# Optimization experiments

Measured on AMD Instinct MI355X. Metric: run time of the kernel, lower is better.

Reference implementation:

```python
import jax, jax.numpy as jnp
import numpy as np

# Routing structure from the torch module
GT0 = [[0,1,0,0,1,0],[0,1,0,0,0,1],[0,0,1,0,1,0],[0,0,1,0,0,1],[0,0,0,1,1,0],[0,0,0,1,0,1]]
NCLS = 6
K = 1  # top-k

def _expert_pairs():
    # For class i, expert index m = 1+(j-1)*5+(k-1) maps to atom1[j-1] -> atom2[k-1].
    pairs = []
    for i in range(NCLS):
        p = [(j - 1, k - 1) for j in range(1, 6) for k in range(1, 6)
             if j != k and GT0[i][j] == 1 and GT0[i][k] == 1]
        pairs.append(p)
    return pairs

PAIRS = _expert_pairs()  # each class has exactly 2 (atom1, atom2) pairs

B, P, D, H = 64, 256, 768, 3072

def setup_inputs() -> dict:
    key = jax.random.key(0)
    ks = jax.random.split(key, 8)
    s = 0.02
    x = jax.random.normal(ks[0], (B, NCLS + P, D), dtype=jnp.float32)
    mids = jax.random.randint(ks[1], (B,), 0, 6)
    moe0_W1 = jax.random.normal(ks[2], (D, H), dtype=jnp.float32) * s
    moe0_b1 = jnp.zeros((H,), jnp.float32)
    moe0_W2 = jax.random.normal(ks[3], (H, D), dtype=jnp.float32) * s
    moe0_b2 = jnp.zeros((D,), jnp.float32)
    A1_W = jax.random.normal(ks[4], (5, D, H), dtype=jnp.float32) * s  # atom1 linears
    A1_b = jnp.zeros((5, H), jnp.float32)
    A2_W = jax.random.normal(ks[5], (5, H, D), dtype=jnp.float32) * s  # atom2 linears
    A2_b = jnp.zeros((5, D), jnp.float32)
    G_W = jax.random.normal(ks[6], (NCLS, D, 2), dtype=jnp.float32) * s  # per-class gates (2 experts each, no bias)
    return {"x": x, "moe0_W1": moe0_W1, "moe0_b1": moe0_b1, "moe0_W2": moe0_W2,
            "moe0_b2": moe0_b2, "A1_W": A1_W, "A1_b": A1_b, "A2_W": A2_W,
            "A2_b": A2_b, "G_W": G_W, "mids": mids}

def _gelu(t):
    return jax.nn.gelu(t, approximate=False)  # torch nn.GELU default = erf

def reference(x, moe0_W1, moe0_b1, moe0_W2, moe0_b2, A1_W, A1_b, A2_W, A2_b, G_W, mids):
    cls_tokens = x[:, :NCLS]          # [B, 6, D]
    patch_tokens = x[:, NCLS:]        # [B, P, D]
    patch_out = _gelu(patch_tokens @ moe0_W1 + moe0_b1) @ moe0_W2 + moe0_b2  # [B, P, D]
    cls_outs = []
    for i in range(NCLS):
        tok = cls_tokens[:, i]        # [B, D]
        eouts = [ _gelu(tok @ A1_W[a] + A1_b[a]) @ A2_W[c] + A2_b[c] for (a, c) in PAIRS[i] ]
        out = jnp.stack(eouts, axis=-1)                 # [B, D, E=2]
        gate = jax.nn.softmax(tok @ G_W[i], axis=-1)    # [B, E]
        # top-k masking (k=1 < E=2): keep gates strictly above the (k+1)-th largest
        thr = jnp.sort(gate, axis=-1)[..., -(K + 1)]    # [B]
        mask = (gate > thr[..., None]).astype(gate.dtype)
        g = gate * mask
        g = g / jnp.clip(jnp.sum(g, axis=-1, keepdims=True), 1e-6)
        cls_outs.append(jnp.sum(out * g[:, None, :], axis=-1))  # [B, D]
    cls_out = jnp.stack(cls_outs, axis=1)               # [B, 6, D]
    return jnp.concatenate([cls_out, patch_out], axis=1)  # [B, 6+P, D]
```

## Files before the change

### kernel.cpp

```cpp
#include <hip/hip_runtime.h>
#include <hip/hip_bf16.h>

#define DD 768
#define HH 3072
#define BB 64
#define TT 262

typedef __bf16 bf16x8 __attribute__((ext_vector_type(8)));
typedef float f32x4 __attribute__((ext_vector_type(4)));
typedef unsigned short u16;
typedef unsigned int u32;

__device__ __constant__ int A_FIRST[12]  = {0,3, 0,4, 1,3, 1,4, 2,3, 2,4};
__device__ __constant__ int A_SECOND[12] = {3,0, 4,0, 3,1, 4,1, 3,2, 4,2};

__device__ __forceinline__ float gelu_f(float x) {
  float n2t = x * fmaf(x * x, -0.0713548163f, -1.5957691216f);
  return x * __builtin_amdgcn_rcpf(1.0f + __expf(n2t));
}

__device__ __forceinline__ u16 f2bf(float x) {
  u32 u = __builtin_bit_cast(u32, x);
  return (u16)((u + 0x7fffu + ((u >> 16) & 1u)) >> 16);
}

__device__ __forceinline__ void load_lds16(const void* g, void* l) {
  __builtin_amdgcn_global_load_lds(
      (const __attribute__((address_space(1))) void*)g,
      (__attribute__((address_space(3))) void*)l,
      16, 0, 0);
}

__global__ __launch_bounds__(256)
void preproc(const float* __restrict__ x,
             const float* __restrict__ W1, const float* __restrict__ A1W,
             const float* __restrict__ W2, const float* __restrict__ A2W,
             const float* __restrict__ GW,
             __hip_bfloat16* __restrict__ xb,
             __hip_bfloat16* __restrict__ W1t, __hip_bfloat16* __restrict__ A1t,
             __hip_bfloat16* __restrict__ W2t, __hip_bfloat16* __restrict__ A2t,
             int* __restrict__ sel) {
  __shared__ __hip_bfloat16 tile[32][33];
  const int bx = blockIdx.x;
  const int tid = threadIdx.x;
  if (bx < 12576) {
    int i = bx * 256 + tid;
    float4 v = ((const float4*)x)[i];
    union { u16 s[4]; uint2 d; } pk;
    pk.s[0] = f2bf(v.x); pk.s[1] = f2bf(v.y); pk.s[2] = f2bf(v.z); pk.s[3] = f2bf(v.w);
    *(uint2*)((u16*)xb + (size_t)i * 4) = pk.d;
  } else if (bx < 40224) {
    int R, C;
    const float* ip;
    __hip_bfloat16* op;
    int t;
    if (bx < 26400) {
      t = bx - 12576; R = DD; C = HH;
      int z = t / 2304; t %= 2304;
      ip = z ? (A1W + (size_t)(z - 1) * DD * HH) : W1;
      op = z ? (A1t + (size_t)(z - 1) * DD * HH) : W1t;
    } else {
      t = bx - 26400; R = HH; C = DD;
      int z = t / 2304; t %= 2304;
      ip = z ? (A2W + (size_t)(z - 1) * DD * HH) : W2;
      op = z ? (A2t + (size_t)(z - 1) * DD * HH) : W2t;
    }
    int ctiles = C >> 5;
    int c0 = (t % ctiles) * 32, r0 = (t / ctiles) * 32;
    int tx = tid & 31, ty = tid >> 5;
#pragma unroll
    for (int s = 0; s < 4; ++s) {
      int rr = ty * 4 + s;
      tile[rr][tx] = __float2bfloat16(ip[(size_t)(r0 + rr) * C + c0 + tx]);
    }
    __syncthreads();
#pragma unroll
    for (int s = 0; s < 4; ++s) {
      int cc = ty * 4 + s;
      op[(size_t)(c0 + cc) * R + r0 + tx] = tile[tx][cc];
    }
  } else {
    int unit = (bx - 40224) * 4 + (tid >> 6);
    int lane = tid & 63;
    int b = unit & 63, i = unit >> 6;
    const float* tok = x + (size_t)(b * TT + i) * DD;
    const float* g = GW + (size_t)i * DD * 2;
    float p0 = 0.f, p1 = 0.f;
    for (int k = lane; k < DD; k += 64) {
      float tv = tok[k];
      p0 += tv * g[k * 2 + 0];
      p1 += tv * g[k * 2 + 1];
    }
#pragma unroll
    for (int o = 32; o; o >>= 1) { p0 += __shfl_xor(p0, o); p1 += __shfl_xor(p1, o); }
    if (lane == 0) sel[i * 64 + b] = (p0 > p1) ? 0 : ((p1 > p0) ? 1 : 2);
  }
}

template <int BM, int BN, int MODE>
__device__ __forceinline__
void gemm_body(char* __restrict__ smem, int bx,
               const __hip_bfloat16* __restrict__ A,
               const __hip_bfloat16* __restrict__ Bw,
               const float* __restrict__ bias,
               void* __restrict__ Out,
               const int* __restrict__ sel) {
  constexpr int KDIM = (MODE == 0 || MODE == 2) ? DD : HH;
  constexpr int KITERS = KDIM / 64;
  constexpr int WAVES_M = (BM == 128) ? 2 : 1;
  constexpr int WAVES_N = 4 / WAVES_M;
  constexpr int MT = BM / (16 * WAVES_M);
  constexpr int NT = BN / (16 * WAVES_N);
  constexpr int CHA = BM / 32;
  constexpr int CHB = BN / 32;

  char* As = smem;
  char* Bs = smem + BM * 128;

  const int tid = threadIdx.x;
  const int lane = tid & 63;
  const int wave = tid >> 6;
  const int q = lane >> 4;
  const int r = lane & 15;
  const int wave_m = wave / WAVES_N;
  const int wave_n = wave % WAVES_N;

  int m0 = 0, n0, combo = 0, cls_i = 0;
  const __hip_bfloat16* Bp = Bw;
  const float* biasp = bias;
  if constexpr (MODE == 0) {
    int chunk = bx / 192, local = bx % 192;
    int nb = local / 16, mloc = local % 16;
    m0 = (chunk * 16 + mloc) * BM;
    n0 = nb * BN;
  } else if constexpr (MODE == 1) {
    int chunk = bx / 96, local = bx % 96;
    int nb = local / 16, mloc = local % 16;
    m0 = (chunk * 16 + mloc) * BM;
    n0 = nb * BN;
  } else if constexpr (MODE == 2) {
    n0 = (bx % 24) * BN;
    combo = bx / 24;
    cls_i = combo >> 1;
    int e = A_FIRST[combo];
    Bp = Bw + (size_t)e * DD * HH;
    biasp = bias + e * HH;
  } else {
    n0 = (bx % 6) * BN;
    combo = bx / 6;
    cls_i = combo >> 1;
    int e = A_SECOND[combo];
    Bp = Bw + (size_t)e * DD * HH;
    biasp = bias + e * DD;
  }

  const int trow = tid >> 3;
  const int sw = ((tid & 7) ^ (trow & 7)) << 4;
  size_t a_row_off;
  if constexpr (MODE == 0) {
    int m = m0 + trow;
    a_row_off = (size_t)((m >> 8) * TT + 6 + (m & 255)) * DD * 2;
  } else if constexpr (MODE == 1) {
    a_row_off = (size_t)(m0 + trow) * HH * 2;
  } else if constexpr (MODE == 2) {
    a_row_off = (size_t)(trow * TT + cls_i) * DD * 2;
  } else {
    a_row_off = (size_t)(combo * 64 + trow) * HH * 2;
  }
  const char* gA0 = (const char*)A + a_row_off + sw;
  const char* gB0 = (const char*)Bp + (size_t)(n0 + trow) * KDIM * 2 + sw;
  constexpr size_t ASTR = (size_t)32 * ((MODE == 0) ? DD : (MODE == 2) ? TT * DD : HH) * 2;
  constexpr size_t BSTR = (size_t)32 * KDIM * 2;
  const int wave_base = (tid & ~63) * 16;

  f32x4 acc[MT][NT];
#pragma unroll
  for (int i_ = 0; i_ < MT; ++i_)
#pragma unroll
    for (int j_ = 0; j_ < NT; ++j_) acc[i_][j_] = (f32x4){0.f, 0.f, 0.f, 0.f};

  const char* a_rd = As + (wave_m * (MT * 16) + r) * 128;
  const char* b_rd = Bs + (wave_n * (NT * 16) + r) * 128;
  const int sa = ((q ^ (r & 7)) << 4);

  for (int kt = 0; kt < KITERS; ++kt) {
#pragma unroll
    for (int u = 0; u < CHA; ++u) load_lds16(gA0 + u * ASTR, As + u * 4096 + wave_base);
#pragma unroll
    for (int u = 0; u < CHB; ++u) load_lds16(gB0 + u * BSTR, Bs + u * 4096 + wave_base);
    gA0 += 128;
    gB0 += 128;
    __syncthreads();
#pragma unroll
    for (int t = 0; t < 2; ++t) {
      const int so = sa ^ (t << 6);
      bf16x8 af[MT], bf[NT];
#pragma unroll
      for (int i_ = 0; i_ < MT; ++i_) af[i_] = *(const bf16x8*)(a_rd + i_ * 2048 + so);
#pragma unroll
      for (int j_ = 0; j_ < NT; ++j_) bf[j_] = *(const bf16x8*)(b_rd + j_ * 2048 + so);
#pragma unroll
      for (int i_ = 0; i_ < MT; ++i_)
#pragma unroll
        for (int j_ = 0; j_ < NT; ++j_)
          acc[i_][j_] = __builtin_amdgcn_mfma_f32_16x16x32_bf16(bf[j_], af[i_], acc[i_][j_], 0, 0, 0);
    }
    __syncthreads();
  }

#pragma unroll
  for (int i_ = 0; i_ < MT; ++i_) {
    int m_g = m0 + wave_m * (MT * 16) + i_ * 16 + r;
#pragma unroll
    for (int j_ = 0; j_ < NT; ++j_) {
      int nb = n0 + wave_n * (NT * 16) + j_ * 16 + q * 4;
      f32x4 v = acc[i_][j_];
      f32x4 bb = *(const f32x4*)(biasp + nb);
      v += bb;
      if constexpr (MODE == 0) {
        union { u16 s[4]; uint2 d; } pk;
#pragma unroll
        for (int rg = 0; rg < 4; ++rg) pk.s[rg] = f2bf(gelu_f(v[rg]));
        *(uint2*)((u16*)Out + (size_t)m_g * HH + nb) = pk.d;
      } else if constexpr (MODE == 1) {
        int b = m_g >> 8, p = m_g & 255;
        *(f32x4*)((float*)Out + (size_t)(b * TT + 6 + p) * DD + nb) = v;
      } else if constexpr (MODE == 2) {
        union { u16 s[4]; uint2 d; } pk;
#pragma unroll
        for (int rg = 0; rg < 4; ++rg) pk.s[rg] = f2bf(gelu_f(v[rg]));
        *(uint2*)((u16*)Out + (size_t)(combo * 64 + m_g) * HH + nb) = pk.d;
      } else {
        int s = sel[cls_i * 64 + m_g];
        int j = combo & 1;
        float* dst = (float*)Out + (size_t)(m_g * TT + cls_i) * DD + nb;
        if (s == j) {
          *(f32x4*)dst = v;
        } else if (j == 0 && s == 2) {
          *(f32x4*)dst = (f32x4){0.f, 0.f, 0.f, 0.f};
        }
      }
    }
  }
}

__global__ __launch_bounds__(256, 2)
void mega1(const __hip_bfloat16* __restrict__ xb, const __hip_bfloat16* __restrict__ W1t,
           const float* __restrict__ b1, __hip_bfloat16* __restrict__ hid,
           const __hip_bfloat16* __restrict__ A1t, const float* __restrict__ A1b,
           __hip_bfloat16* __restrict__ hcls) {
  __shared__ __align__(16) char smem[(128 + 256) * 128];
  int bx = blockIdx.x;
  if (bx < 1536) gemm_body<128, 256, 0>(smem, bx, xb, W1t, b1, hid, nullptr);
  else           gemm_body<64, 128, 2>(smem, bx - 1536, xb, A1t, A1b, hcls, nullptr);
}

__global__ __launch_bounds__(256, 2)
void mega2(const __hip_bfloat16* __restrict__ hid, const __hip_bfloat16* __restrict__ W2t,
           const float* __restrict__ b2, float* __restrict__ out,
           const __hip_bfloat16* __restrict__ hcls, const __hip_bfloat16* __restrict__ A2t,
           const float* __restrict__ A2b, const int* __restrict__ sel) {
  __shared__ __align__(16) char smem[(128 + 128) * 128];
  int bx = blockIdx.x;
  if (bx < 768) gemm_body<128, 128, 1>(smem, bx, hid, W2t, b2, out, nullptr);
  else          gemm_body<64, 128, 3>(smem, bx - 768, hcls, A2t, A2b, out, sel);
}

extern "C" void kernel_launch(void* const* d_in, const int* in_sizes, int n_in,
                              void* d_out, int out_size, void* d_ws, size_t ws_size,
                              hipStream_t stream) {
  const float* x   = (const float*)d_in[0];
  const float* W1  = (const float*)d_in[1];
  const float* b1  = (const float*)d_in[2];
  const float* W2  = (const float*)d_in[3];
  const float* b2  = (const float*)d_in[4];
  const float* A1W = (const float*)d_in[5];
  const float* A1b = (const float*)d_in[6];
  const float* A2W = (const float*)d_in[7];
  const float* A2b = (const float*)d_in[8];
  const float* GW  = (const float*)d_in[9];
  float* out = (float*)d_out;

  char* ws = (char*)d_ws;
  __hip_bfloat16* xb   = (__hip_bfloat16*)(ws + 0);
  __hip_bfloat16* W1t  = (__hip_bfloat16*)(ws + 25755648);
  __hip_bfloat16* W2t  = (__hip_bfloat16*)(ws + 30474240);
  __hip_bfloat16* A1t  = (__hip_bfloat16*)(ws + 35192832);
  __hip_bfloat16* A2t  = (__hip_bfloat16*)(ws + 58785792);
  __hip_bfloat16* hcls = (__hip_bfloat16*)(ws + 82378752);
  int* sel             = (int*)(ws + 87097344);
  __hip_bfloat16* hid  = (__hip_bfloat16*)(ws + 87099136);

  preproc<<<40320, 256, 0, stream>>>(x, W1, A1W, W2, A2W, GW, xb, W1t, A1t, W2t, A2t, sel);
  mega1<<<1824, 256, 0, stream>>>(xb, W1t, b1, hid, A1t, A1b, hcls);
  mega2<<<840, 256, 0, stream>>>(hid, W2t, b2, out, hcls, A2t, A2b, sel);
}
```

Before: 403.0 us.

## Use 256x256 double-buffered GEMM tiles with interleaved LDS staging and MFMA

Replaces the generic GEMM body for the two large patch GEMMs with a 512-thread, 256x256-tile kernel. It double-buffers LDS (128KB) and interleaves the next K-slab's global-to-LDS loads with MFMA groups, using vmcnt waits, raw barriers and s_setprio. The goal is to hide global load latency and raise data reuse per tile. The small class-token GEMMs get their own 512-thread path. The trade-offs: the second GEMM now launches only 192 large tiles, which may leave CUs idle, and the large LDS footprint limits occupancy to one block per CU.

```diff
diff --git a/kernel.cpp b/kernel.cpp
--- a/kernel.cpp
+++ b/kernel.cpp
@@ -30,6 +30,9 @@
       (__attribute__((address_space(3))) void*)l,
       16, 0, 0);
 }
+
+#define VMCNT(n) asm volatile("s_waitcnt vmcnt(" #n ")")
+#define BAR() __builtin_amdgcn_s_barrier()
 
 __global__ __launch_bounds__(256)
 void preproc(const float* __restrict__ x,
@@ -97,173 +100,265 @@
   }
 }
 
-template <int BM, int BN, int MODE>
+template <int MH, int KS>
+__device__ __forceinline__ void rd_a(bf16x8 (&af)[4], const char* ab, int a_rd0) {
+#pragma unroll
+  for (int ii = 0; ii < 4; ++ii)
+    af[ii] = *(const bf16x8*)(ab + MH * 16384 + ii * 2048 + (a_rd0 ^ (KS << 6)));
+}
+template <int KS>
+__device__ __forceinline__ void rd_b(bf16x8 (&bf)[4], const char* bb, int b_rd0) {
+#pragma unroll
+  for (int j = 0; j < 4; ++j)
+    bf[j] = *(const bf16x8*)(bb + (j >> 1) * 16384 + (j & 1) * 2048 + (b_rd0 ^ (KS << 6)));
+}
+template <int MH>
+__device__ __forceinline__ void mma16(f32x4 (&acc)[8][4], const bf16x8 (&af)[4], const bf16x8 (&bf)[4]) {
+  __builtin_amdgcn_s_setprio(1);
+#pragma unroll
+  for (int ii = 0; ii < 4; ++ii)
+#pragma unroll
+    for (int j = 0; j < 4; ++j)
+      acc[MH * 4 + ii][j] =
+          __builtin_amdgcn_mfma_f32_16x16x32_bf16(bf[j], af[ii], acc[MH * 4 + ii][j], 0, 0, 0);
+  __builtin_amdgcn_s_setprio(0);
+}
+
+template <int MODE>
 __device__ __forceinline__
-void gemm_body(char* __restrict__ smem, int bx,
-               const __hip_bfloat16* __restrict__ A,
-               const __hip_bfloat16* __restrict__ Bw,
-               const float* __restrict__ bias,
-               void* __restrict__ Out,
-               const int* __restrict__ sel) {
-  constexpr int KDIM = (MODE == 0 || MODE == 2) ? DD : HH;
-  constexpr int KITERS = KDIM / 64;
-  constexpr int WAVES_M = (BM == 128) ? 2 : 1;
-  constexpr int WAVES_N = 4 / WAVES_M;
-  constexpr int MT = BM / (16 * WAVES_M);
-  constexpr int NT = BN / (16 * WAVES_N);
-  constexpr int CHA = BM / 32;
-  constexpr int CHB = BN / 32;
+void gemm_big(char* __restrict__ smem, int bx,
+              const __hip_bfloat16* __restrict__ A,
+              const __hip_bfloat16* __restrict__ Bw,
+              const float* __restrict__ bias,
+              void* __restrict__ Out) {
+  constexpr int KDIM = (MODE == 0) ? DD : HH;
+  constexpr int KT = KDIM / 64;
+  constexpr int KB = KDIM * 2;
 
   char* As = smem;
-  char* Bs = smem + BM * 128;
+  char* Bs = smem + 65536;
 
   const int tid = threadIdx.x;
   const int lane = tid & 63;
-  const int wave = tid >> 6;
   const int q = lane >> 4;
   const int r = lane & 15;
-  const int wave_m = wave / WAVES_N;
-  const int wave_n = wave % WAVES_N;
-
-  int m0 = 0, n0, combo = 0, cls_i = 0;
-  const __hip_bfloat16* Bp = Bw;
-  const float* biasp = bias;
+  const int wave = tid >> 6;
+  const int wave_m = wave >> 2;
+  const int wave_n = wave & 3;
+
+  int m0, n0;
   if constexpr (MODE == 0) {
     int chunk = bx / 192, local = bx % 192;
-    int nb = local / 16, mloc = local % 16;
-    m0 = (chunk * 16 + mloc) * BM;
-    n0 = nb * BN;
-  } else if constexpr (MODE == 1) {
-    int chunk = bx / 96, local = bx % 96;
-    int nb = local / 16, mloc = local % 16;
-    m0 = (chunk * 16 + mloc) * BM;
-    n0 = nb * BN;
-  } else if constexpr (MODE == 2) {
-    n0 = (bx % 24) * BN;
-    combo = bx / 24;
-    cls_i = combo >> 1;
-    int e = A_FIRST[combo];
-    Bp = Bw + (size_t)e * DD * HH;
-    biasp = bias + e * HH;
+    m0 = (chunk * 16 + local % 16) * 256;
+    n0 = (local / 16) * 256;
   } else {
-    n0 = (bx % 6) * BN;
-    combo = bx / 6;
-    cls_i = combo >> 1;
-    int e = A_SECOND[combo];
-    Bp = Bw + (size_t)e * DD * HH;
-    biasp = bias + e * DD;
+    m0 = (bx % 64) * 256;
+    n0 = (bx / 64) * 256;
   }
 
   const int trow = tid >> 3;
   const int sw = ((tid & 7) ^ (trow & 7)) << 4;
-  size_t a_row_off;
-  if constexpr (MODE == 0) {
-    int m = m0 + trow;
-    a_row_off = (size_t)((m >> 8) * TT + 6 + (m & 255)) * DD * 2;
-  } else if constexpr (MODE == 1) {
-    a_row_off = (size_t)(m0 + trow) * HH * 2;
-  } else if constexpr (MODE == 2) {
-    a_row_off = (size_t)(trow * TT + cls_i) * DD * 2;
-  } else {
-    a_row_off = (size_t)(combo * 64 + trow) * HH * 2;
-  }
-  const char* gA0 = (const char*)A + a_row_off + sw;
-  const char* gB0 = (const char*)Bp + (size_t)(n0 + trow) * KDIM * 2 + sw;
-  constexpr size_t ASTR = (size_t)32 * ((MODE == 0) ? DD : (MODE == 2) ? TT * DD : HH) * 2;
-  constexpr size_t BSTR = (size_t)32 * KDIM * 2;
-  const int wave_base = (tid & ~63) * 16;
-
-  f32x4 acc[MT][NT];
-#pragma unroll
-  for (int i_ = 0; i_ < MT; ++i_)
-#pragma unroll
-    for (int j_ = 0; j_ < NT; ++j_) acc[i_][j_] = (f32x4){0.f, 0.f, 0.f, 0.f};
-
-  const char* a_rd = As + (wave_m * (MT * 16) + r) * 128;
-  const char* b_rd = Bs + (wave_n * (NT * 16) + r) * 128;
-  const int sa = ((q ^ (r & 7)) << 4);
-
-  for (int kt = 0; kt < KITERS; ++kt) {
-#pragma unroll
-    for (int u = 0; u < CHA; ++u) load_lds16(gA0 + u * ASTR, As + u * 4096 + wave_base);
-#pragma unroll
-    for (int u = 0; u < CHB; ++u) load_lds16(gB0 + u * BSTR, Bs + u * 4096 + wave_base);
-    gA0 += 128;
-    gB0 += 128;
-    __syncthreads();
-#pragma unroll
-    for (int t = 0; t < 2; ++t) {
-      const int so = sa ^ (t << 6);
-      bf16x8 af[MT], bf[NT];
-#pragma unroll
-      for (int i_ = 0; i_ < MT; ++i_) af[i_] = *(const bf16x8*)(a_rd + i_ * 2048 + so);
-#pragma unroll
-      for (int j_ = 0; j_ < NT; ++j_) bf[j_] = *(const bf16x8*)(b_rd + j_ * 2048 + so);
-#pragma unroll
-      for (int i_ = 0; i_ < MT; ++i_)
-#pragma unroll
-        for (int j_ = 0; j_ < NT; ++j_)
-          acc[i_][j_] = __builtin_amdgcn_mfma_f32_16x16x32_bf16(bf[j_], af[i_], acc[i_][j_], 0, 0, 0);
-    }
-    __syncthreads();
-  }
-
-#pragma unroll
-  for (int i_ = 0; i_ < MT; ++i_) {
-    int m_g = m0 + wave_m * (MT * 16) + i_ * 16 + r;
-#pragma unroll
-    for (int j_ = 0; j_ < NT; ++j_) {
-      int nb = n0 + wave_n * (NT * 16) + j_ * 16 + q * 4;
-      f32x4 v = acc[i_][j_];
-      f32x4 bb = *(const f32x4*)(biasp + nb);
-      v += bb;
+  size_t a_row;
+  if constexpr (MODE == 0) a_row = (size_t)((m0 >> 8) * TT + 6 + trow);
+  else                     a_row = (size_t)(m0 + trow);
+  const char* gA = (const char*)A + a_row * KB + sw;
+  const char* gB = (const char*)Bw + (size_t)(n0 + trow) * KB + sw;
+  const int ldsb = (tid & ~63) * 16;
+
+#define STAGE_A(h, kt, bsel) do { \
+    load_lds16(gA + (size_t)((h) * 128) * KB + (kt) * 128,      As + ((bsel) << 15) + (h) * 16384 + ldsb); \
+    load_lds16(gA + (size_t)((h) * 128 + 64) * KB + (kt) * 128, As + ((bsel) << 15) + (h) * 16384 + 8192 + ldsb); \
+  } while (0)
+#define STAGE_B(h, kt, bsel) do { \
+    load_lds16(gB + (size_t)((h) * 128) * KB + (kt) * 128,      Bs + ((bsel) << 15) + (h) * 16384 + ldsb); \
+    load_lds16(gB + (size_t)((h) * 128 + 64) * KB + (kt) * 128, Bs + ((bsel) << 15) + (h) * 16384 + 8192 + ldsb); \
+  } while (0)
+
+  const int a_rd0 = (wave_m * 64 + r) * 128 + ((q ^ (r & 7)) << 4);
+  const int b_rd0 = (wave_n * 32 + r) * 128 + ((q ^ (r & 7)) << 4);
+
+  f32x4 acc[8][4];
+#pragma unroll
+  for (int i = 0; i < 8; ++i)
+#pragma unroll
+    for (int j = 0; j < 4; ++j) acc[i][j] = (f32x4){0.f, 0.f, 0.f, 0.f};
+  bf16x8 af[4], bf0[4], bf1[4];
+
+  STAGE_A(0, 0, 0); STAGE_B(0, 0, 0); STAGE_B(1, 0, 0); STAGE_A(1, 0, 0);
+  VMCNT(2);
+  BAR();
+
+  for (int t = 0; t < KT - 1; ++t) {
+    const int bsel = t & 1, nsel = bsel ^ 1;
+    const char* ab = As + (bsel << 15);
+    const char* bb = Bs + (bsel << 15);
+    rd_a<0, 0>(af, ab, a_rd0);
+    rd_b<0>(bf0, bb, b_rd0);
+    STAGE_A(0, t + 1, nsel);
+    BAR();
+    mma16<0>(acc, af, bf0);
+    BAR();
+    rd_a<0, 1>(af, ab, a_rd0);
+    rd_b<1>(bf1, bb, b_rd0);
+    STAGE_B(0, t + 1, nsel);
+    BAR();
+    mma16<0>(acc, af, bf1);
+    VMCNT(4);
+    BAR();
+    rd_a<1, 0>(af, ab, a_rd0);
+    STAGE_B(1, t + 1, nsel);
+    BAR();
+    mma16<1>(acc, af, bf0);
+    BAR();
+    rd_a<1, 1>(af, ab, a_rd0);
+    STAGE_A(1, t + 1, nsel);
+    BAR();
+    mma16<1>(acc, af, bf1);
+    VMCNT(2);
+    BAR();
+  }
+  {
+    const char* ab = As + (((KT - 1) & 1) << 15);
+    const char* bb = Bs + (((KT - 1) & 1) << 15);
+    rd_a<0, 0>(af, ab, a_rd0);
+    rd_b<0>(bf0, bb, b_rd0);
+    BAR(); mma16<0>(acc, af, bf0); BAR();
+    rd_a<0, 1>(af, ab, a_rd0);
+    rd_b<1>(bf1, bb, b_rd0);
+    BAR(); mma16<0>(acc, af, bf1);
+    VMCNT(0);
+    BAR();
+    rd_a<1, 0>(af, ab, a_rd0);
+    BAR(); mma16<1>(acc, af, bf0); BAR();
+    rd_a<1, 1>(af, ab, a_rd0);
+    BAR(); mma16<1>(acc, af, bf1);
+  }
+#undef STAGE_A
+#undef STAGE_B
+
+#pragma unroll
+  for (int i = 0; i < 8; ++i) {
+    const int m_g = m0 + (i >> 2) * 128 + wave_m * 64 + (i & 3) * 16 + r;
+#pragma unroll
+    for (int j = 0; j < 4; ++j) {
+      const int n_g = n0 + (j >> 1) * 128 + wave_n * 32 + (j & 1) * 16 + q * 4;
+      f32x4 v = acc[i][j];
+      v += *(const f32x4*)(bias + n_g);
       if constexpr (MODE == 0) {
         union { u16 s[4]; uint2 d; } pk;
 #pragma unroll
         for (int rg = 0; rg < 4; ++rg) pk.s[rg] = f2bf(gelu_f(v[rg]));
-        *(uint2*)((u16*)Out + (size_t)m_g * HH + nb) = pk.d;
-      } else if constexpr (MODE == 1) {
-        int b = m_g >> 8, p = m_g & 255;
-        *(f32x4*)((float*)Out + (size_t)(b * TT + 6 + p) * DD + nb) = v;
-      } else if constexpr (MODE == 2) {
+        *(uint2*)((u16*)Out + (size_t)m_g * HH + n_g) = pk.d;
+      } else {
+        const int b = m_g >> 8, p = m_g & 255;
+        *(f32x4*)((float*)Out + (size_t)(b * TT + 6 + p) * DD + n_g) = v;
+      }
+    }
+  }
+}
+
+template <int MODE>
+__device__ __forceinline__
+void gemm_cls(char* __restrict__ smem, int bx,
+              const __hip_bfloat16* __restrict__ A,
+              const __hip_bfloat16* __restrict__ Bw,
+              const float* __restrict__ bias,
+              void* __restrict__ Out, const int* __restrict__ sel) {
+  constexpr int KDIM = (MODE == 2) ? DD : HH;
+  constexpr int KT = KDIM / 64;
+  char* As = smem;
+  char* Bs = smem + 8192;
+
+  const int tid = threadIdx.x;
+  const int lane = tid & 63;
+  const int q = lane >> 4;
+  const int r = lane & 15;
+  const int wave = tid >> 6;
+  const int wave_m = wave >> 2;
+  const int wave_n = wave & 3;
+
+  int n0, combo, e;
+  if constexpr (MODE == 2) { n0 = (bx % 24) * 128; combo = bx / 24; e = A_FIRST[combo]; }
+  else                     { n0 = (bx % 6) * 128;  combo = bx / 6;  e = A_SECOND[combo]; }
+  const int cls_i = combo >> 1;
+  const __hip_bfloat16* Bp = Bw + (size_t)e * DD * HH;
+  const float* biasp = bias + e * ((MODE == 2) ? HH : DD);
+
+  const int trow = tid >> 3;
+  const int sw = ((tid & 7) ^ (trow & 7)) << 4;
+  const char* gA = (const char*)A +
+      ((MODE == 2) ? (size_t)(trow * TT + cls_i) * (DD * 2)
+                   : (size_t)(combo * 64 + trow) * (HH * 2)) + sw;
+  const char* gB = (const char*)Bp + (size_t)(n0 + trow) * (KDIM * 2) + sw;
+  const int ldsb = (tid & ~63) * 16;
+  const int sa = (q ^ (r & 7)) << 4;
+
+  f32x4 acc[2][2];
+  acc[0][0] = acc[0][1] = acc[1][0] = acc[1][1] = (f32x4){0.f, 0.f, 0.f, 0.f};
+
+  for (int t = 0; t < KT; ++t) {
+    load_lds16(gA + t * 128, As + ldsb);
+    load_lds16(gB + t * 128, Bs + ldsb);
+    load_lds16(gB + (size_t)64 * (KDIM * 2) + t * 128, Bs + 8192 + ldsb);
+    __syncthreads();
+#pragma unroll
+    for (int ks = 0; ks < 2; ++ks) {
+      bf16x8 a0 = *(const bf16x8*)(As + (wave_m * 32 + r) * 128 + (sa ^ (ks << 6)));
+      bf16x8 a1 = *(const bf16x8*)(As + (wave_m * 32 + 16 + r) * 128 + (sa ^ (ks << 6)));
+      bf16x8 b0 = *(const bf16x8*)(Bs + (wave_n * 32 + r) * 128 + (sa ^ (ks << 6)));
+      bf16x8 b1 = *(const bf16x8*)(Bs + (wave_n * 32 + 16 + r) * 128 + (sa ^ (ks << 6)));
+      acc[0][0] = __builtin_amdgcn_mfma_f32_16x16x32_bf16(b0, a0, acc[0][0], 0, 0, 0);
+      acc[0][1] = __builtin_amdgcn_mfma_f32_16x16x32_bf16(b1, a0, acc[0][1], 0, 0, 0);
+      acc[1][0] = __builtin_amdgcn_mfma_f32_16x16x32_bf16(b0, a1, acc[1][0], 0, 0, 0);
+      acc[1][1] = __builtin_amdgcn_mfma_f32_16x16x32_bf16(b1, a1, acc[1][1], 0, 0, 0);
+    }
+    __syncthreads();
+  }
+
+#pragma unroll
+  for (int i = 0; i < 2; ++i) {
+    const int m_g = wave_m * 32 + i * 16 + r;
+#pragma unroll
+    for (int j = 0; j < 2; ++j) {
+      const int n_g = n0 + wave_n * 32 + j * 16 + q * 4;
+      f32x4 v = acc[i][j];
+      v += *(const f32x4*)(biasp + n_g);
+      if constexpr (MODE == 2) {
         union { u16 s[4]; uint2 d; } pk;
 #pragma unroll
         for (int rg = 0; rg < 4; ++rg) pk.s[rg] = f2bf(gelu_f(v[rg]));
-        *(uint2*)((u16*)Out + (size_t)(combo * 64 + m_g) * HH + nb) = pk.d;
+        *(uint2*)((u16*)Out + (size_t)(combo * 64 + m_g) * HH + n_g) = pk.d;
       } else {
-        int s = sel[cls_i * 64 + m_g];
-        int j = combo & 1;
-        float* dst = (float*)Out + (size_t)(m_g * TT + cls_i) * DD + nb;
-        if (s == j) {
-          *(f32x4*)dst = v;
-        } else if (j == 0 && s == 2) {
-          *(f32x4*)dst = (f32x4){0.f, 0.f, 0.f, 0.f};
-        }
+        const int s = sel[cls_i * 64 + m_g];
+        const int jj = combo & 1;
+        float* dst = (float*)Out + (size_t)(m_g * TT + cls_i) * DD + n_g;
+        if (s == jj)                    *(f32x4*)dst = v;
+        else if (jj == 0 && s == 2)     *(f32x4*)dst = (f32x4){0.f, 0.f, 0.f, 0.f};
       }
     }
   }
 }
 
-__global__ __launch_bounds__(256, 2)
+__global__ __launch_bounds__(512, 2)
 void mega1(const __hip_bfloat16* __restrict__ xb, const __hip_bfloat16* __restrict__ W1t,
            const float* __restrict__ b1, __hip_bfloat16* __restrict__ hid,
            const __hip_bfloat16* __restrict__ A1t, const float* __restrict__ A1b,
            __hip_bfloat16* __restrict__ hcls) {
-  __shared__ __align__(16) char smem[(128 + 256) * 128];
+  __shared__ __align__(16) char smem[131072];
   int bx = blockIdx.x;
-  if (bx < 1536) gemm_body<128, 256, 0>(smem, bx, xb, W1t, b1, hid, nullptr);
-  else           gemm_body<64, 128, 2>(smem, bx - 1536, xb, A1t, A1b, hcls, nullptr);
-}
-
-__global__ __launch_bounds__(256, 2)
+  if (bx < 768) gemm_big<0>(smem, bx, xb, W1t, b1, hid);
+  else          gemm_cls<2>(smem, bx - 768, xb, A1t, A1b, hcls, nullptr);
+}
+
+__global__ __launch_bounds__(512, 2)
 void mega2(const __hip_bfloat16* __restrict__ hid, const __hip_bfloat16* __restrict__ W2t,
            const float* __restrict__ b2, float* __restrict__ out,
            const __hip_bfloat16* __restrict__ hcls, const __hip_bfloat16* __restrict__ A2t,
            const float* __restrict__ A2b, const int* __restrict__ sel) {
-  __shared__ __align__(16) char smem[(128 + 128) * 128];
+  __shared__ __align__(16) char smem[131072];
   int bx = blockIdx.x;
-  if (bx < 768) gemm_body<128, 128, 1>(smem, bx, hid, W2t, b2, out, nullptr);
-  else          gemm_body<64, 128, 3>(smem, bx - 768, hcls, A2t, A2b, out, sel);
+  if (bx < 192) gemm_big<1>(smem, bx, hid, W2t, b2, out);
+  else          gemm_cls<3>(smem, bx - 192, hcls, A2t, A2b, out, sel);
 }
 
 extern "C" void kernel_launch(void* const* d_in, const int* in_sizes, int n_in,
@@ -292,6 +387,6 @@
   __hip_bfloat16* hid  = (__hip_bfloat16*)(ws + 87099136);
 
   preproc<<<40320, 256, 0, stream>>>(x, W1, A1W, W2, A2W, GW, xb, W1t, A1t, W2t, A2t, sel);
-  mega1<<<1824, 256, 0, stream>>>(xb, W1t, b1, hid, A1t, A1b, hcls);
-  mega2<<<840, 256, 0, stream>>>(hid, W2t, b2, out, hcls, A2t, A2b, sel);
-}
+  mega1<<<1056, 512, 0, stream>>>(xb, W1t, b1, hid, A1t, A1b, hcls);
+  mega2<<<264, 512, 0, stream>>>(hid, W2t, b2, out, hcls, A2t, A2b, sel);
+}
```

After: 398.6 us. Within noise of the previous version (-1.1%).
